# Kernel optimization log

Hardware: AMD Instinct MI355X
Metric: run time of the kernel (lower is better)

## Reference

```python
import jax, jax.numpy as jnp
import numpy as np

K = 3; PAD = 1; STRIDE = 1; EPS = 1e-5


def setup_inputs() -> dict:
    key = jax.random.key(0)
    k0, k1, k2 = jax.random.split(key, 3)
    B, C, H, W, O = 4, 256, 64, 64, 256
    x = jax.random.normal(k0, (B, C, H, W), jnp.float32)
    # offset conv: small random weights so offsets are nontrivial but bounded
    w_off = jax.random.normal(k1, (2 * K * K, C, K, K), jnp.float32) * 0.01
    b_off = jnp.zeros((2 * K * K,), jnp.float32)
    # kaiming normal, mode=fan_out: std = sqrt(2 / (O*K*K))
    w_def = jax.random.normal(k2, (O, C, K, K), jnp.float32) * np.float32(np.sqrt(2.0 / (O * K * K)))
    gamma = jnp.ones((O,), jnp.float32)
    beta = jnp.zeros((O,), jnp.float32)
    return {"x": x, "w_off": w_off, "b_off": b_off, "w_def": w_def, "gamma": gamma, "beta": beta}


def _bilinear_gather(x, py, px):
    """x: [B,C,H,W]; py,px: [B,K2,Ho,Wo] float sample coords.
    Returns [B,K2,Ho,Wo,C] with zero padding outside (per-corner masking,
    matching torchvision deform_conv2d)."""
    B, C, H, W = x.shape
    y0f = jnp.floor(py); x0f = jnp.floor(px)
    wy1 = py - y0f; wy0 = 1.0 - wy1
    wx1 = px - x0f; wx0 = 1.0 - wx1
    bidx = jnp.arange(B)[:, None, None, None]

    def corner(yf, xf, wgt):
        valid = (yf >= 0) & (yf <= H - 1) & (xf >= 0) & (xf <= W - 1)
        yc = jnp.clip(yf.astype(jnp.int32), 0, H - 1)
        xc = jnp.clip(xf.astype(jnp.int32), 0, W - 1)
        v = x[bidx, :, yc, xc]  # [B,K2,Ho,Wo,C] (advanced idx moves C last)
        return v * (wgt * valid)[..., None]

    return (corner(y0f, x0f, wy0 * wx0) + corner(y0f, x0f + 1.0, wy0 * wx1)
            + corner(y0f + 1.0, x0f, wy1 * wx0) + corner(y0f + 1.0, x0f + 1.0, wy1 * wx1))


def _forward(x, w_off, b_off, w_def, gamma, beta):
    B, C, H, W = x.shape
    O = w_def.shape[0]
    K2 = K * K
    # 1) offset-predicting conv
    off = jax.lax.conv_general_dilated(x, w_off, (STRIDE, STRIDE), ((PAD, PAD), (PAD, PAD)))
    off = off + b_off[None, :, None, None]
    Ho, Wo = off.shape[2], off.shape[3]
    off = off.reshape(B, K2, 2, Ho, Wo)  # pairs (dy, dx) per kernel tap
    # 2) deformable sampling locations
    ky, kx = jnp.meshgrid(jnp.arange(K, dtype=jnp.float32), jnp.arange(K, dtype=jnp.float32), indexing='ij')
    base_y = (jnp.arange(Ho, dtype=jnp.float32) * STRIDE - PAD)
    base_x = (jnp.arange(Wo, dtype=jnp.float32) * STRIDE - PAD)
    py = off[:, :, 0] + ky.reshape(K2)[None, :, None, None] + base_y[None, None, :, None]
    px = off[:, :, 1] + kx.reshape(K2)[None, :, None, None] + base_x[None, None, None, :]
    vals = _bilinear_gather(x, py, px)  # [B,K2,Ho,Wo,C]
    # 3) deform conv GEMM (bias=False)
    out = jnp.einsum('bkhwc,ock->bohw', vals, w_def.reshape(O, C, K2))
    # 4) BatchNorm (training mode: batch stats) + ReLU
    mean = out.mean(axis=(0, 2, 3))
    var = out.var(axis=(0, 2, 3))
    out = (out - mean[None, :, None, None]) * (gamma * jax.lax.rsqrt(var + EPS))[None, :, None, None]
    out = out + beta[None, :, None, None]
    return jax.nn.relu(out)


def reference(x, w_off, b_off, w_def, gamma, beta):
    return _forward(x, w_off, b_off, w_def, gamma, beta)
```

## Files before the change

### kernel.cpp

```cpp
#include <hip/hip_runtime.h>
#include <hip/hip_bf16.h>

typedef unsigned int  uint;
typedef unsigned short ushort;
typedef short bf16x8 __attribute__((ext_vector_type(8)));
typedef float f32x4  __attribute__((ext_vector_type(4)));

#define HW   4096
#define KD   2304

__device__ __forceinline__ void load_lds16(const void* g, void* l) {
    __builtin_amdgcn_global_load_lds((const __attribute__((address_space(1))) void*)g,
                                     (__attribute__((address_space(3))) void*)l, 16, 0, 0);
}
__device__ __forceinline__ float blo(uint u) { return __uint_as_float(u << 16); }
__device__ __forceinline__ float bhi(uint u) { return __uint_as_float(u & 0xffff0000u); }
__device__ __forceinline__ uint pack2(float e, float o) {
    __hip_bfloat16 he = __float2bfloat16(e), ho = __float2bfloat16(o);
    return (uint)(*(ushort*)&he) | ((uint)(*(ushort*)&ho) << 16);
}

__global__ void prep_x2t(const float* __restrict__ x, uint* __restrict__ x2t) {
    __shared__ uint tl[32][65];
    int bidx = blockIdx.x;
    int ab  = bidx & 63;
    int cpb = (bidx >> 6) & 3;
    int b   = bidx >> 8;
    int t = threadIdx.x;
#pragma unroll
    for (int i = 0; i < 8; ++i) {
        int idx = i * 256 + t;
        int cp = idx >> 6, a = idx & 63;
        const float* p = x + ((size_t)(b * 256 + (cpb * 32 + cp) * 2)) * HW + ab * 64 + a;
        tl[cp][a] = pack2(p[0], p[HW]);
    }
    __syncthreads();
#pragma unroll
    for (int i = 0; i < 8; ++i) {
        int idx = i * 256 + t;
        int a = idx >> 5, cp = idx & 31;
        x2t[((size_t)b * 4096 + ab * 64 + a) * 128 + cpb * 32 + cp] = tl[cp][a];
    }
}

__global__ void prep_bt(const float* __restrict__ w_def, ushort* __restrict__ bt) {
    int idx = blockIdx.x * 256 + threadIdx.x;
    int c   = idx & 255;
    int tap = (idx >> 8) % 9;
    int o   = idx / KD;
    __hip_bfloat16 h = __float2bfloat16(w_def[(o * 256 + c) * 9 + tap]);
    bt[idx] = *(ushort*)&h;
}

__global__ void prep_bt0(const float* __restrict__ w_off, ushort* __restrict__ bt0) {
    int idx = blockIdx.x * 256 + threadIdx.x;
    int c   = idx & 255;
    int tap = (idx >> 8) % 9;
    int j   = idx / KD;
    float v = (j < 18) ? w_off[(j * 256 + c) * 9 + tap] : 0.f;
    __hip_bfloat16 h = __float2bfloat16(v);
    bt0[idx] = *(ushort*)&h;
}

__global__ __launch_bounds__(512) void gemm_off(const uint* __restrict__ x2t,
                                                const ushort* __restrict__ bt0,
                                                const float* __restrict__ b_off,
                                                float* __restrict__ off) {
    int id = blockIdx.x;
    int xcd = id & 7;
    int b = xcd >> 1, h = (xcd & 1) * 32 + (id >> 3);
    int t = threadIdx.x, wv = t >> 6, lane = t & 63;
    int mrow = lane & 15, quad = lane >> 4;
    int mq = wv & 3, nn = wv >> 2;

    __shared__ uint   lX[3 * 64 * 32];
    __shared__ ushort lB[32 * 576];

    f32x4 acc = {0.f, 0.f, 0.f, 0.f};

    for (int cb = 0; cb < 4; ++cb) {
#pragma unroll
        for (int s = 0; s < 3; ++s) {
            int q   = s * 8 + wv;
            int dy  = q >> 3;
            int y   = h + dy - 1;
            int sub = q & 7;
            int wl  = sub * 8 + (lane >> 3);
            int cps = ((lane & 7) ^ ((lane >> 3) & 7)) * 4;
            if ((unsigned)y < 64u) {
                const uint* src = x2t + ((size_t)(b * 4096 + y * 64 + wl)) * 128 + cb * 32 + cps;
                load_lds16(src, &lX[q * 256]);
            } else {
                uint4 z = {0u, 0u, 0u, 0u};
                *(uint4*)&lX[q * 256 + lane * 4] = z;
            }
        }
#pragma unroll
        for (int s = 0; s < 5; ++s) {
            int q = s * 8 + wv;
            if (q < 36) {
                int e = q * 512 + lane * 8;
                int o  = e / 576;
                int r  = e - o * 576;
                int chp = r >> 3;
                int ch  = chp ^ (o & 7);
                int tap = ch >> 3, k8 = ch & 7;
                const ushort* src = bt0 + (size_t)o * KD + tap * 256 + cb * 64 + k8 * 8;
                load_lds16(src, &lB[q * 512]);
            }
        }
        __syncthreads();

#pragma unroll
        for (int tap = 0; tap < 9; ++tap) {
            int dy = tap / 3, dx = tap % 3;
            int xx = mq * 16 + mrow + dx - 1;
            bool vx = (unsigned)xx < 64u;
            int xc = min(max(xx, 0), 63);
#pragma unroll
            for (int kb = 0; kb < 2; ++kb) {
                int cp0 = kb * 16 + quad * 4;
                uint4 ad = {0u, 0u, 0u, 0u};
                if (vx) ad = *(const uint4*)&lX[dy * 2048 + xc * 32 + (cp0 ^ ((xc & 7) * 4))];
                bf16x8 af = *(bf16x8*)&ad;
                int o = nn * 16 + mrow;
                int chs = (tap * 8 + (((kb * 4 + quad)) ^ (o & 7)));
                bf16x8 bfr = *(const bf16x8*)&lB[o * 576 + chs * 8];
                acc = __builtin_amdgcn_mfma_f32_16x16x32_bf16(af, bfr, acc, 0, 0, 0);
            }
        }
        __syncthreads();
    }
    {
        int o = nn * 16 + mrow;
        float bias = (o < 18) ? b_off[o] : 0.f;
        f32x4 v = acc;
        v.x += bias; v.y += bias; v.z += bias; v.w += bias;
        int wpos = mq * 16 + quad * 4;
        *(f32x4*)(off + ((size_t)(b * 32 + o)) * HW + h * 64 + wpos) = v;
    }
}

__global__ __launch_bounds__(1024, 4) void fused_main(const uint* __restrict__ x2t,
                                                      const ushort* __restrict__ bt,
                                                      const float* __restrict__ off,
                                                      float* __restrict__ out,
                                                      float* __restrict__ stats) {
    int id = blockIdx.x;
    int xcd = id & 7;
    int b = xcd >> 1, h = (xcd & 1) * 32 + (id >> 3);
    int t = threadIdx.x;
    int wv = t >> 6, lane = t & 63;
    int mrow = lane & 15, quad = lane >> 4;
    bool producer = (wv < 8);
    int w  = t & 63;
    int cq = (t >> 6) & 7;

    __shared__ int    sAc[4][9][64];
    __shared__ float  sWc[4][9][64];
    __shared__ ushort lA[2][64 * 64];
    __shared__ ushort lB[2][256 * 64];

    for (int i = t; i < 576; i += 1024) {
        int tap = i >> 6, ww = i & 63;
        int hw = h * 64 + ww;
        float oy = off[((size_t)(b * 32 + 2 * tap)) * HW + hw];
        float ox = off[((size_t)(b * 32 + 2 * tap + 1)) * HW + hw];
        float py = oy + (float)(tap / 3 + h - 1);
        float px = ox + (float)(tap % 3 + ww - 1);
        float y0f = floorf(py), x0f = floorf(px);
        float wy1 = py - y0f, wx1 = px - x0f;
        float wy0 = 1.f - wy1, wx0 = 1.f - wx1;
        bool vy0 = (y0f >= 0.f) && (y0f <= 63.f);
        bool vy1 = (y0f >= -1.f) && (y0f <= 62.f);
        bool vx0 = (x0f >= 0.f) && (x0f <= 63.f);
        bool vx1 = (x0f >= -1.f) && (x0f <= 62.f);
        int iy0 = min(max((int)y0f, 0), 63),  iy1 = min(max((int)y0f + 1, 0), 63);
        int ix0 = min(max((int)x0f, 0), 63),  ix1 = min(max((int)x0f + 1, 0), 63);
        sAc[0][tap][ww] = iy0 * 64 + ix0;
        sAc[1][tap][ww] = iy0 * 64 + ix1;
        sAc[2][tap][ww] = iy1 * 64 + ix0;
        sAc[3][tap][ww] = iy1 * 64 + ix1;
        sWc[0][tap][ww] = wy0 * wx0 * (float)(vy0 && vx0);
        sWc[1][tap][ww] = wy0 * wx1 * (float)(vy0 && vx1);
        sWc[2][tap][ww] = wy1 * wx0 * (float)(vy1 && vx0);
        sWc[3][tap][ww] = wy1 * wx1 * (float)(vy1 && vx1);
    }
    __syncthreads();

    f32x4 acc[4][2];
#pragma unroll
    for (int m = 0; m < 4; ++m)
#pragma unroll
        for (int n = 0; n < 2; ++n) acc[m][n] = {0.f, 0.f, 0.f, 0.f};

    const uint* xb = x2t + (size_t)b * 4096 * 128;

    auto stage = [&](int sl, ushort* lAb, ushort* lBb) {
        int tap = sl >> 2, cb = sl & 3;
        int a0 = sAc[0][tap][w], a1 = sAc[1][tap][w], a2 = sAc[2][tap][w], a3 = sAc[3][tap][w];
        float f0 = sWc[0][tap][w], f1 = sWc[1][tap][w], f2 = sWc[2][tap][w], f3 = sWc[3][tap][w];
        const uint* xp = xb + cb * 32 + cq * 4;
        uint4 v0 = *(const uint4*)(xp + (size_t)a0 * 128);
        uint4 v1 = *(const uint4*)(xp + (size_t)a1 * 128);
        uint4 v2 = *(const uint4*)(xp + (size_t)a2 * 128);
        uint4 v3 = *(const uint4*)(xp + (size_t)a3 * 128);
#pragma unroll
        for (int s2 = 0; s2 < 4; ++s2) {
            int e = s2 * 512 + t;
            int o = e >> 3, pp = e & 7;
            int k8 = pp ^ (o & 7);
            const ushort* src = bt + (size_t)o * KD + tap * 256 + cb * 64 + k8 * 8;
            load_lds16(src, &lBb[(e & ~63) * 8]);
        }
        const uint* c0 = (const uint*)&v0;
        const uint* c1 = (const uint*)&v1;
        const uint* c2 = (const uint*)&v2;
        const uint* c3 = (const uint*)&v3;
        uint r[4];
#pragma unroll
        for (int j = 0; j < 4; ++j) {
            float ev = f0 * blo(c0[j]) + f1 * blo(c1[j]) + f2 * blo(c2[j]) + f3 * blo(c3[j]);
            float ov = f0 * bhi(c0[j]) + f1 * bhi(c1[j]) + f2 * bhi(c2[j]) + f3 * bhi(c3[j]);
            r[j] = pack2(ev, ov);
        }
        uint4 g = {r[0], r[1], r[2], r[3]};
        *(uint4*)&lAb[w * 64 + ((cq ^ (w & 7)) * 8)] = g;
    };

    if (producer) stage(0, lA[0], lB[0]);

    int p = 0;
    for (int s = 0; s < 36; ++s) {
        __syncthreads();
        if (producer) {
            if (s + 1 < 36) stage(s + 1, lA[p ^ 1], lB[p ^ 1]);
        } else {
            int wvc = wv - 8;
#pragma unroll
            for (int kb = 0; kb < 2; ++kb) {
                bf16x8 af[4];
#pragma unroll
                for (int m = 0; m < 4; ++m) {
                    int r = m * 16 + mrow;
                    af[m] = *(const bf16x8*)&lA[p][r * 64 + (((kb * 4 + quad) ^ (r & 7)) * 8)];
                }
#pragma unroll
                for (int n = 0; n < 2; ++n) {
                    int r = wvc * 32 + n * 16 + mrow;
                    bf16x8 bfr = *(const bf16x8*)&lB[p][r * 64 + (((kb * 4 + quad) ^ (r & 7)) * 8)];
#pragma unroll
                    for (int m = 0; m < 4; ++m)
                        acc[m][n] = __builtin_amdgcn_mfma_f32_16x16x32_bf16(af[m], bfr, acc[m][n], 0, 0, 0);
                }
            }
        }
        p ^= 1;
    }

    if (!producer) {
        int wvc = wv - 8;
#pragma unroll
        for (int n = 0; n < 2; ++n) {
            int o = wvc * 32 + n * 16 + mrow;
            float ss = 0.f, qq = 0.f;
#pragma unroll
            for (int m = 0; m < 4; ++m) {
                int pos = m * 16 + quad * 4;
                f32x4 v = acc[m][n];
                *(f32x4*)(out + ((size_t)(b * 256 + o)) * HW + h * 64 + pos) = v;
                ss += v.x + v.y + v.z + v.w;
                qq += v.x * v.x + v.y * v.y + v.z * v.z + v.w * v.w;
            }
            ss += __shfl_xor(ss, 16); ss += __shfl_xor(ss, 32);
            qq += __shfl_xor(qq, 16); qq += __shfl_xor(qq, 32);
            if (quad == 0) {
                atomicAdd(&stats[o], ss);
                atomicAdd(&stats[512 + o], qq);
            }
        }
    }
}

__global__ void bn_finalize(const float* __restrict__ stats,
                            const float* __restrict__ gamma,
                            float* __restrict__ ms) {
    int o = threadIdx.x;
    float S = stats[o], S2 = stats[512 + o];
    float m  = S / 16384.f;
    float var = S2 / 16384.f - m * m;
    ms[o]       = m;
    ms[256 + o] = gamma[o] * rsqrtf(var + 1e-5f);
}

__global__ void bn_apply(float* __restrict__ out,
                         const float* __restrict__ ms,
                         const float* __restrict__ beta) {
    int idx4 = blockIdx.x * 256 + threadIdx.x;
    int o = (idx4 >> 10) & 255;
    float4 v = ((const float4*)out)[idx4];
    float mu = ms[o], sc = ms[256 + o], be = beta[o];
    v.x = fmaxf((v.x - mu) * sc + be, 0.f);
    v.y = fmaxf((v.y - mu) * sc + be, 0.f);
    v.z = fmaxf((v.z - mu) * sc + be, 0.f);
    v.w = fmaxf((v.w - mu) * sc + be, 0.f);
    ((float4*)out)[idx4] = v;
}

extern "C" void kernel_launch(void* const* d_in, const int* in_sizes, int n_in,
                              void* d_out, int out_size, void* d_ws, size_t ws_size,
                              hipStream_t stream) {
    const float* x     = (const float*)d_in[0];
    const float* w_off = (const float*)d_in[1];
    const float* b_off = (const float*)d_in[2];
    const float* w_def = (const float*)d_in[3];
    const float* gamma = (const float*)d_in[4];
    const float* beta  = (const float*)d_in[5];
    float* out = (float*)d_out;

    char* ws = (char*)d_ws;
    uint*   x2t   = (uint*)ws;
    ushort* bt    = (ushort*)(ws + 8388608);
    ushort* bt0   = (ushort*)(ws + 9568256);
    float*  off   = (float*)(ws + 9715712);
    float*  stats = (float*)(ws + 11812864);
    float*  ms    = (float*)(ws + 11816960);

    hipMemsetAsync(stats, 0, 4096, stream);
    prep_x2t<<<1024, 256, 0, stream>>>(x, x2t);
    prep_bt <<<2304, 256, 0, stream>>>(w_def, bt);
    prep_bt0<<<288,  256, 0, stream>>>(w_off, bt0);
    gemm_off<<<256, 512, 0, stream>>>(x2t, bt0, b_off, off);
    fused_main<<<256, 1024, 0, stream>>>(x2t, bt, off, out, stats);
    bn_finalize<<<1, 256, 0, stream>>>(stats, gamma, ms);
    bn_apply<<<4096, 256, 0, stream>>>(out, ms, beta);
}
```

Before: 165.9 us.

## Prefetch deformable gathers one stage ahead in producer waves

Producer waves now issue the four bilinear corner gathers for the next-but-one K slice into registers before finishing the current slice. The blend and LDS write then run on data already in flight, hiding global gather latency. The loop is unrolled by two with fixed buffer indices, and the thread-to-(position, channel chunk) mapping changes so each wave covers 8 positions by 8 channel chunks instead of 64 positions by one chunk. This costs extra VGPRs for two sets of gather registers under a launch bound of 1024 threads with 4 blocks per multiprocessor, which may cause spills.

```diff
diff --git a/kernel.cpp b/kernel.cpp
--- a/kernel.cpp
+++ b/kernel.cpp
@@ -153,8 +153,8 @@
     int wv = t >> 6, lane = t & 63;
     int mrow = lane & 15, quad = lane >> 4;
     bool producer = (wv < 8);
-    int w  = t & 63;
-    int cq = (t >> 6) & 7;
+    int ppos = (wv << 3) + (lane >> 3);
+    int pc8  = lane & 7;
 
     __shared__ int    sAc[4][9][64];
     __shared__ float  sWc[4][9][64];
@@ -196,15 +196,16 @@
 
     const uint* xb = x2t + (size_t)b * 4096 * 128;
 
-    auto stage = [&](int sl, ushort* lAb, ushort* lBb) {
+    auto issue_gathers = [&](int sl, uint4 (&g)[4]) {
         int tap = sl >> 2, cb = sl & 3;
-        int a0 = sAc[0][tap][w], a1 = sAc[1][tap][w], a2 = sAc[2][tap][w], a3 = sAc[3][tap][w];
-        float f0 = sWc[0][tap][w], f1 = sWc[1][tap][w], f2 = sWc[2][tap][w], f3 = sWc[3][tap][w];
-        const uint* xp = xb + cb * 32 + cq * 4;
-        uint4 v0 = *(const uint4*)(xp + (size_t)a0 * 128);
-        uint4 v1 = *(const uint4*)(xp + (size_t)a1 * 128);
-        uint4 v2 = *(const uint4*)(xp + (size_t)a2 * 128);
-        uint4 v3 = *(const uint4*)(xp + (size_t)a3 * 128);
+        const uint* xp = xb + cb * 32 + pc8 * 4;
+        g[0] = *(const uint4*)(xp + (size_t)sAc[0][tap][ppos] * 128);
+        g[1] = *(const uint4*)(xp + (size_t)sAc[1][tap][ppos] * 128);
+        g[2] = *(const uint4*)(xp + (size_t)sAc[2][tap][ppos] * 128);
+        g[3] = *(const uint4*)(xp + (size_t)sAc[3][tap][ppos] * 128);
+    };
+    auto issue_B = [&](int sl, ushort* lBb) {
+        int tap = sl >> 2, cb = sl & 3;
 #pragma unroll
         for (int s2 = 0; s2 < 4; ++s2) {
             int e = s2 * 512 + t;
@@ -213,10 +214,15 @@
             const ushort* src = bt + (size_t)o * KD + tap * 256 + cb * 64 + k8 * 8;
             load_lds16(src, &lBb[(e & ~63) * 8]);
         }
-        const uint* c0 = (const uint*)&v0;
-        const uint* c1 = (const uint*)&v1;
-        const uint* c2 = (const uint*)&v2;
-        const uint* c3 = (const uint*)&v3;
+    };
+    auto finish = [&](int sl, ushort* lAb, const uint4 (&g)[4]) {
+        int tap = sl >> 2;
+        float f0 = sWc[0][tap][ppos], f1 = sWc[1][tap][ppos];
+        float f2 = sWc[2][tap][ppos], f3 = sWc[3][tap][ppos];
+        const uint* c0 = (const uint*)&g[0];
+        const uint* c1 = (const uint*)&g[1];
+        const uint* c2 = (const uint*)&g[2];
+        const uint* c3 = (const uint*)&g[3];
         uint r[4];
 #pragma unroll
         for (int j = 0; j < 4; ++j) {
@@ -224,38 +230,57 @@
             float ov = f0 * bhi(c0[j]) + f1 * bhi(c1[j]) + f2 * bhi(c2[j]) + f3 * bhi(c3[j]);
             r[j] = pack2(ev, ov);
         }
-        uint4 g = {r[0], r[1], r[2], r[3]};
-        *(uint4*)&lAb[w * 64 + ((cq ^ (w & 7)) * 8)] = g;
+        uint4 gg = {r[0], r[1], r[2], r[3]};
+        *(uint4*)&lAb[ppos * 64 + ((pc8 ^ (ppos & 7)) * 8)] = gg;
     };
-
-    if (producer) stage(0, lA[0], lB[0]);
-
-    int p = 0;
-    for (int s = 0; s < 36; ++s) {
+    auto mfma_pass = [&](int bi) {
+        int wvc = wv - 8;
+#pragma unroll
+        for (int kb = 0; kb < 2; ++kb) {
+            bf16x8 af[4];
+#pragma unroll
+            for (int m = 0; m < 4; ++m) {
+                int r = m * 16 + mrow;
+                af[m] = *(const bf16x8*)&lA[bi][r * 64 + (((kb * 4 + quad) ^ (r & 7)) * 8)];
+            }
+#pragma unroll
+            for (int n = 0; n < 2; ++n) {
+                int r = wvc * 32 + n * 16 + mrow;
+                bf16x8 bfr = *(const bf16x8*)&lB[bi][r * 64 + (((kb * 4 + quad) ^ (r & 7)) * 8)];
+#pragma unroll
+                for (int m = 0; m < 4; ++m)
+                    acc[m][n] = __builtin_amdgcn_mfma_f32_16x16x32_bf16(af[m], bfr, acc[m][n], 0, 0, 0);
+            }
+        }
+    };
+
+    uint4 gA[4], gB[4];
+    if (producer) {
+        issue_gathers(0, gA);
+        issue_B(0, lB[0]);
+        finish(0, lA[0], gA);
+        issue_gathers(1, gB);
+    }
+
+    for (int s = 0; s < 36; s += 2) {
         __syncthreads();
         if (producer) {
-            if (s + 1 < 36) stage(s + 1, lA[p ^ 1], lB[p ^ 1]);
+            issue_B(s + 1, lB[1]);
+            if (s + 2 < 36) issue_gathers(s + 2, gA);
+            finish(s + 1, lA[1], gB);
         } else {
-            int wvc = wv - 8;
-#pragma unroll
-            for (int kb = 0; kb < 2; ++kb) {
-                bf16x8 af[4];
-#pragma unroll
-                for (int m = 0; m < 4; ++m) {
-                    int r = m * 16 + mrow;
-                    af[m] = *(const bf16x8*)&lA[p][r * 64 + (((kb * 4 + quad) ^ (r & 7)) * 8)];
-                }
-#pragma unroll
-                for (int n = 0; n < 2; ++n) {
-                    int r = wvc * 32 + n * 16 + mrow;
-                    bf16x8 bfr = *(const bf16x8*)&lB[p][r * 64 + (((kb * 4 + quad) ^ (r & 7)) * 8)];
-#pragma unroll
-                    for (int m = 0; m < 4; ++m)
-                        acc[m][n] = __builtin_amdgcn_mfma_f32_16x16x32_bf16(af[m], bfr, acc[m][n], 0, 0, 0);
-                }
-            }
-        }
-        p ^= 1;
+            mfma_pass(0);
+        }
+        __syncthreads();
+        if (producer) {
+            if (s + 2 < 36) {
+                issue_B(s + 2, lB[0]);
+                if (s + 3 < 36) issue_gathers(s + 3, gB);
+                finish(s + 2, lA[0], gA);
+            }
+        } else {
+            mfma_pass(1);
+        }
     }
 
     if (!producer) {
```

Result: no change. 168.4 us (+1.5%).
